# Kernel optimization log

Measured on AMD Instinct MI355X. Metric: run time of the kernel, lower is better.

## Reference

```python
import jax, jax.numpy as jnp
import numpy as np

EMB, HID, VOC, NLAYERS, TLEN = 256, 512, 32000, 2, 64
SRC_LEN, BS = 128, 64
DEC_HID = 2 * HID  # decoder hidden = hidden_dim * 2


def _p(key, shape, scale=0.05):
    return jax.random.normal(key, shape, dtype=jnp.float32) * scale


def setup_inputs() -> dict:
    key = jax.random.key(0)
    ks = jax.random.split(key, 24)
    d = {}
    d["sentences"] = jax.random.randint(ks[0], (SRC_LEN, BS), 0, VOC)
    d["targets"] = jax.random.randint(ks[1], (TLEN, BS), 0, VOC)
    d["emb"] = _p(ks[2], (VOC, EMB))
    # encoder: bidirectional, 2 layers; gate order i,f,g,o (PyTorch)
    d["enc0_Wih"] = _p(ks[3], (2, 4 * HID, EMB))
    d["enc0_Whh"] = _p(ks[4], (2, 4 * HID, HID))
    d["enc0_bih"] = _p(ks[5], (2, 4 * HID))
    d["enc0_bhh"] = _p(ks[6], (2, 4 * HID))
    d["enc1_Wih"] = _p(ks[7], (2, 4 * HID, 2 * HID))
    d["enc1_Whh"] = _p(ks[8], (2, 4 * HID, HID))
    d["enc1_bih"] = _p(ks[9], (2, 4 * HID))
    d["enc1_bhh"] = _p(ks[10], (2, 4 * HID))
    # decoder: unidirectional, 2 layers, hidden DEC_HID
    d["dec0_Wih"] = _p(ks[11], (4 * DEC_HID, EMB))
    d["dec0_Whh"] = _p(ks[12], (4 * DEC_HID, DEC_HID))
    d["dec0_bih"] = _p(ks[13], (4 * DEC_HID,))
    d["dec0_bhh"] = _p(ks[14], (4 * DEC_HID,))
    d["dec1_Wih"] = _p(ks[15], (4 * DEC_HID, DEC_HID))
    d["dec1_Whh"] = _p(ks[16], (4 * DEC_HID, DEC_HID))
    d["dec1_bih"] = _p(ks[17], (4 * DEC_HID,))
    d["dec1_bhh"] = _p(ks[18], (4 * DEC_HID,))
    d["W_out"] = _p(ks[19], (VOC, DEC_HID))
    d["b_out"] = _p(ks[20], (VOC,))
    return d


def lstm_scan(x, h0, c0, Wih, Whh, bih, bhh, reverse=False):
    # x: (T,B,In). Precompute input projection for the whole sequence.
    xw = jnp.einsum('tbi,gi->tbg', x, Wih) + bih  # (T,B,4H)

    def step(carry, g_in):
        h, c = carry
        g = g_in + h @ Whh.T + bhh
        i, f, gg, o = jnp.split(g, 4, axis=-1)
        c = jax.nn.sigmoid(f) * c + jax.nn.sigmoid(i) * jnp.tanh(gg)
        h = jax.nn.sigmoid(o) * jnp.tanh(c)
        return (h, c), h

    (hT, cT), ys = jax.lax.scan(step, (h0, c0), xw, reverse=reverse)
    return ys, hT, cT


def _forward(sentences, targets, emb,
             enc0_Wih, enc0_Whh, enc0_bih, enc0_bhh,
             enc1_Wih, enc1_Whh, enc1_bih, enc1_bhh,
             dec0_Wih, dec0_Whh, dec0_bih, dec0_bhh,
             dec1_Wih, dec1_Whh, dec1_bih, dec1_bhh,
             W_out, b_out):
    bs = sentences.shape[1]
    x = emb[sentences]  # (S,B,E)
    z = jnp.zeros((bs, HID), jnp.float32)
    enc_layers = ((enc0_Wih, enc0_Whh, enc0_bih, enc0_bhh),
                  (enc1_Wih, enc1_Whh, enc1_bih, enc1_bhh))
    hs, cs = [], []
    for Wih, Whh, bih, bhh in enc_layers:
        yf, hf, cf = lstm_scan(x, z, z, Wih[0], Whh[0], bih[0], bhh[0])
        yb, hb, cb = lstm_scan(x, z, z, Wih[1], Whh[1], bih[1], bhh[1], reverse=True)
        x = jnp.concatenate([yf, yb], axis=-1)  # (S,B,2H)
        hs.append(jnp.concatenate([hf, hb], axis=-1))  # _reshape_hidden concat
        cs.append(jnp.concatenate([cf, cb], axis=-1))
    # teacher forcing: decoder inputs are last source token, then targets[:-1]
    dec_tokens = jnp.concatenate([sentences[-1:], targets[:-1]], axis=0)  # (T,B)
    y = emb[dec_tokens]  # (T,B,E); dropout is identity in eval mode
    dec_layers = ((dec0_Wih, dec0_Whh, dec0_bih, dec0_bhh),
                  (dec1_Wih, dec1_Whh, dec1_bih, dec1_bhh))
    for l, (Wih, Whh, bih, bhh) in enumerate(dec_layers):
        y, _, _ = lstm_scan(y, hs[l], cs[l], Wih, Whh, bih, bhh)
    logits = jnp.einsum('tbh,vh->tbv', y, W_out) + b_out  # (T,B,V)
    return jax.nn.log_softmax(logits, axis=-1)


def reference(sentences, targets, emb,
              enc0_Wih, enc0_Whh, enc0_bih, enc0_bhh,
              enc1_Wih, enc1_Whh, enc1_bih, enc1_bhh,
              dec0_Wih, dec0_Whh, dec0_bih, dec0_bhh,
              dec1_Wih, dec1_Whh, dec1_bih, dec1_bhh,
              W_out, b_out):
    return _forward(sentences, targets, emb,
                    enc0_Wih, enc0_Whh, enc0_bih, enc0_bhh,
                    enc1_Wih, enc1_Whh, enc1_bih, enc1_bhh,
                    dec0_Wih, dec0_Whh, dec0_bih, dec0_bhh,
                    dec1_Wih, dec1_Whh, dec1_bih, dec1_bhh,
                    W_out, b_out)
```

## Files before the change

kernel.cpp:

```cpp
#include <hip/hip_runtime.h>

#define S_LEN 128
#define T_LEN 64
#define BSZ   64
#define EMBD  256
#define HID_  512
#define DHID_ 1024
#define VOC_  32000
#define HSTR  1024

typedef float  f4_t  __attribute__((ext_vector_type(4)));
typedef float  f32x4 __attribute__((ext_vector_type(4)));
typedef short  s16x8 __attribute__((ext_vector_type(8)));
typedef __bf16 bf16x8 __attribute__((ext_vector_type(8)));
typedef unsigned short u16x4 __attribute__((ext_vector_type(4)));
typedef int    i32x2 __attribute__((ext_vector_type(2)));

#define WS_XWA  0ull
#define WS_XWB  (WS_XWA + 16777216ull)
#define WS_CS   (WS_XWB + 16777216ull)
#define WS_BAR  (WS_CS  + 131072ull)
#define WS_BF   (WS_BAR + 32768ull)
#define U_X0B   0ull
#define U_HE0   (U_X0B + 2097152ull)
#define U_HE1   (U_HE0 + 8388608ull)
#define U_HD0   (U_HE1 + 8388608ull)
#define U_HD1   (U_HD0 + 4194304ull)
#define U_HSB   (U_HD1 + 4194304ull)
#define U_E0W   (U_HSB + 131072ull)
#define U_E1W   (U_E0W + 1048576ull)
#define U_D0W   (U_E1W + 4194304ull)
#define U_D1W   (U_D0W + 1048576ull)

__device__ __forceinline__ unsigned short f2bf(float x) {
    unsigned u = __builtin_bit_cast(unsigned, x);
    return (unsigned short)((u + 0x7fffu + ((u >> 16) & 1u)) >> 16);
}

__device__ __forceinline__ f4_t sc_load4(const void* p) {
    f4_t v;
    asm volatile("global_load_dwordx4 %0, %1, off sc0 sc1" : "=v"(v) : "v"(p));
    return v;
}
__device__ __forceinline__ int sc_load1(const int* p) {
    int v;
    asm volatile("global_load_dword %0, %1, off sc0 sc1\n\ts_waitcnt vmcnt(0)"
                 : "=v"(v) : "v"(p) : "memory");
    return v;
}
__device__ __forceinline__ void sc_store_int(int* p, int v) {
    asm volatile("global_store_dword %0, %1, off sc0 sc1" :: "v"(p), "v"(v) : "memory");
}
__device__ __forceinline__ void sc_store8(void* p, i32x2 v) {
    asm volatile("global_store_dwordx2 %0, %1, off sc0 sc1" :: "v"(p), "v"(v) : "memory");
}
__device__ __forceinline__ float g_load1(const float* p) {
    float v;
    asm volatile("global_load_dword %0, %1, off" : "=v"(v) : "v"(p));
    return v;
}
__device__ __forceinline__ void wait_vm0() {
    asm volatile("s_waitcnt vmcnt(0)" ::: "memory");
}
__device__ __forceinline__ void wait_vm8() {
    asm volatile("s_waitcnt vmcnt(8)" ::: "memory");
}

__device__ __forceinline__ void gload_lds16(const void* g, void* l) {
    __builtin_amdgcn_global_load_lds(
        (const __attribute__((address_space(1))) void*)g,
        (__attribute__((address_space(3))) void*)l, 16, 0, 0);
}

__device__ __forceinline__ float sigmoidf_(float x) { return 1.f / (1.f + expf(-x)); }

__global__ __launch_bounds__(256) void f2b_kernel(
    const float* __restrict__ in, unsigned short* __restrict__ out, int n4)
{
    const int stride = gridDim.x * 256;
    for (int i = blockIdx.x * 256 + threadIdx.x; i < n4; i += stride) {
        const float4 v = reinterpret_cast<const float4*>(in)[i];
        u16x4 o = { f2bf(v.x), f2bf(v.y), f2bf(v.z), f2bf(v.w) };
        reinterpret_cast<u16x4*>(out)[i] = o;
    }
}

__global__ __launch_bounds__(64) void embed_src_kernel(
    const int* __restrict__ toks, const float* __restrict__ emb,
    unsigned short* __restrict__ out)
{
    const int i = blockIdx.x;
    const int tok = toks[i];
    const float4 v = reinterpret_cast<const float4*>(emb + (size_t)tok * EMBD)[threadIdx.x];
    u16x4 o = { f2bf(v.x), f2bf(v.y), f2bf(v.z), f2bf(v.w) };
    reinterpret_cast<u16x4*>(out + (size_t)i * EMBD)[threadIdx.x] = o;
}

__global__ __launch_bounds__(64) void embed_dec_kernel(
    const int* __restrict__ sent, const int* __restrict__ targ,
    const float* __restrict__ emb, unsigned short* __restrict__ out)
{
    const int i = blockIdx.x;
    const int t = i >> 6, b = i & 63;
    const int tok = (t == 0) ? sent[(S_LEN - 1) * BSZ + b] : targ[(t - 1) * BSZ + b];
    const float4 v = reinterpret_cast<const float4*>(emb + (size_t)tok * EMBD)[threadIdx.x];
    u16x4 o = { f2bf(v.x), f2bf(v.y), f2bf(v.z), f2bf(v.w) };
    reinterpret_cast<u16x4*>(out + (size_t)i * EMBD)[threadIdx.x] = o;
}

__global__ __launch_bounds__(256) void gemm_bf16_kernel(
    const unsigned short* __restrict__ A, const unsigned short* __restrict__ B,
    const float* __restrict__ b1, const float* __restrict__ b2,
    float* __restrict__ C, int M, int N, int K, int nTN, int tmode)
{
    __shared__ __align__(16) unsigned short As[128 * 64];
    __shared__ __align__(16) unsigned short Bs[128 * 64];

    const int tid  = threadIdx.x;
    const int lane = tid & 63;
    const int wv   = tid >> 6;
    const int wm   = wv >> 1, wn = wv & 1;

    const int nwg = gridDim.x;
    const int q = nwg >> 3, r = nwg & 7;
    const int xcd = blockIdx.x & 7, io = blockIdx.x >> 3;
    const int wg = (xcd < r ? xcd * (q + 1) : r * (q + 1) + (xcd - r) * q) + io;
    const int bm = (wg / nTN) * 128;
    const int bn = (wg % nTN) * 128;

    f32x4 acc[4][4];
#pragma unroll
    for (int i = 0; i < 4; ++i)
#pragma unroll
        for (int j = 0; j < 4; ++j) acc[i][j] = (f32x4)0.f;

    const int lin_base = wv * 1024 + lane * 16;

    for (int k0 = 0; k0 < K; k0 += 64) {
        __syncthreads();
#pragma unroll
        for (int qc = 0; qc < 4; ++qc) {
            const int lin = qc * 4096 + lin_base;
            const int row = lin >> 7;
            const int c   = (lin >> 4) & 7;
            const int sc  = c ^ (row & 7);
            const size_t gofs  = (size_t)(bm + row) * K + k0 + sc * 8;
            const size_t gofsB = (size_t)(bn + row) * K + k0 + sc * 8;
            char* ldst  = (char*)As + qc * 4096 + wv * 1024;
            char* ldstB = (char*)Bs + qc * 4096 + wv * 1024;
            gload_lds16(A + gofs, ldst);
            gload_lds16(B + gofsB, ldstB);
        }
        asm volatile("s_waitcnt vmcnt(0)" ::: "memory");
        __syncthreads();
#pragma unroll
        for (int ks = 0; ks < 2; ++ks) {
            bf16x8 af[4], bfv[4];
            const int ca = ks * 4 + (lane >> 4);
#pragma unroll
            for (int f = 0; f < 4; ++f) {
                const int ra = wm * 64 + f * 16 + (lane & 15);
                af[f] = __builtin_bit_cast(bf16x8,
                    *(const s16x8*)((const char*)As + ra * 128 + ((ca ^ (ra & 7)) << 4)));
                const int rb = wn * 64 + f * 16 + (lane & 15);
                bfv[f] = __builtin_bit_cast(bf16x8,
                    *(const s16x8*)((const char*)Bs + rb * 128 + ((ca ^ (rb & 7)) << 4)));
            }
#pragma unroll
            for (int i = 0; i < 4; ++i)
#pragma unroll
                for (int j = 0; j < 4; ++j)
                    acc[i][j] = __builtin_amdgcn_mfma_f32_16x16x32_bf16(
                        af[i], bfv[j], acc[i][j], 0, 0, 0);
        }
    }

    const int col0 = bn + wn * 64 + (lane & 15);
    if (tmode == 0) {
        const int row0 = bm + wm * 64 + ((lane >> 4) << 2);
#pragma unroll
        for (int i = 0; i < 4; ++i) {
#pragma unroll
            for (int j = 0; j < 4; ++j) {
                const int col = col0 + j * 16;
                float bias = b1[col];
                if (b2) bias += b2[col];
#pragma unroll
                for (int rg = 0; rg < 4; ++rg)
                    C[(size_t)(row0 + i * 16 + rg) * N + col] = acc[i][j][rg] + bias;
            }
        }
    } else {
        const int tblk = (bm >> 6) + wm;
        const int rb = (lane >> 4) << 2;
#pragma unroll
        for (int i = 0; i < 4; ++i) {
#pragma unroll
            for (int j = 0; j < 4; ++j) {
                const int col = col0 + j * 16;
                float bias = b1[col];
                if (b2) bias += b2[col];
                float4 v = { acc[i][j][0] + bias, acc[i][j][1] + bias,
                             acc[i][j][2] + bias, acc[i][j][3] + bias };
                *reinterpret_cast<float4*>(&C[((size_t)tblk * N + col) * 64 + rb + i * 16]) = v;
            }
        }
    }
}

template<int H_T>
__global__ __launch_bounds__(256, 1) void lstm_mfma_scan(
    const float* __restrict__ xw0, const float* __restrict__ xw1,
    const float* __restrict__ Whh0, const float* __restrict__ Whh1,
    const unsigned short* __restrict__ h0b, const float* __restrict__ c0,
    unsigned short* __restrict__ hist,
    unsigned short* __restrict__ hsb, float* __restrict__ csd,
    int T, int ndir, int rev_mask, int* bar)
{
    constexpr int KST = H_T / 32;
    constexpr int CH  = H_T / 8;
    constexpr int NB  = (64 * CH) / 2048;

    __shared__ __align__(16) unsigned short h_lds[64 * H_T];
    __shared__ float pre[64][17];
    __shared__ __align__(8) unsigned short hpack[64][4];

    const int tid  = threadIdx.x;
    const int lane = tid & 63;
    const int w    = tid >> 6;
    const int bpd  = (ndir == 2) ? 128 : 256;
    const int dir  = blockIdx.x / bpd;
    const int blk  = blockIdx.x - dir * bpd;
    const int m0   = blk * 4;
    const int rev  = (rev_mask >> dir) & 1;
    const float* xw  = dir ? xw1  : xw0;
    const float* Whh = dir ? Whh1 : Whh0;
    const int dcol = dir * H_T;
    const int b = tid & 63;
    const int j = tid >> 6;

    int* myflag = bar + blockIdx.x * 32;
    const int* pollflag = bar + (dir * bpd + (tid < bpd ? tid : 0)) * 32;
    const bool polls = (tid < bpd);

    const int n  = lane & 15;
    const int kg = lane >> 4;
    const int wr = (n >> 2) * H_T + m0 + (n & 3);
    s16x8 wfr[KST];
#pragma unroll
    for (int ks = 0; ks < KST; ++ks) {
        const float* wp = Whh + (size_t)wr * H_T + ks * 32 + kg * 8;
        const float4 lo = *reinterpret_cast<const float4*>(wp);
        const float4 hi = *reinterpret_cast<const float4*>(wp + 4);
        s16x8 rr;
        rr[0] = (short)f2bf(lo.x); rr[1] = (short)f2bf(lo.y);
        rr[2] = (short)f2bf(lo.z); rr[3] = (short)f2bf(lo.w);
        rr[4] = (short)f2bf(hi.x); rr[5] = (short)f2bf(hi.y);
        rr[6] = (short)f2bf(hi.z); rr[7] = (short)f2bf(hi.w);
        wfr[ks] = rr;
    }

    float c  = c0 ? c0[(size_t)b * HSTR + dcol + m0 + j] : 0.f;
    float hn = 0.f;
    const int rA  = w * 16 + n;
    const int rAx = rA & 7;

    for (int s = 0; s < T; ++s) {
        const int tt = rev ? (T - 1 - s) : s;

        const float* xb = xw + ((size_t)tt * (4 * H_T) + m0 + j) * 64 + b;
        float xg0 = g_load1(xb);
        float xg1 = g_load1(xb + (size_t)H_T * 64);
        float xg2 = g_load1(xb + (size_t)2 * H_T * 64);
        float xg3 = g_load1(xb + (size_t)3 * H_T * 64);

        if (s > 0) {
            int ok = polls ? 0 : 1;
            for (;;) {
                if (!ok) ok = (sc_load1(pollflag) >= s) ? 1 : 0;
                if (__syncthreads_and(ok)) break;
            }
        }

        const unsigned short* hb;
        size_t tofs;
        if (s == 0) { hb = h0b; tofs = 0; }
        else {
            const int tp = rev ? (tt + 1) : (tt - 1);
            hb = hist; tofs = (size_t)tp * (64 * 1024);
        }

        float p0 = 0.f, p1 = 0.f, p2 = 0.f, p3 = 0.f;
        if (hb) {
            f4_t bufA[8], bufB[8];
            auto issue = [&](f4_t (&bf)[8], int bt) {
#pragma unroll
                for (int jj = 0; jj < 8; ++jj) {
                    const int idx = (bt * 8 + jj) * 256 + tid;
                    const int rr_ = idx / CH, cc_ = idx % CH;
                    bf[jj] = sc_load4(hb + tofs + (size_t)rr_ * 1024 + dcol + cc_ * 8);
                }
            };
            auto writeb = [&](const f4_t (&bf)[8], int bt) {
#pragma unroll
                for (int jj = 0; jj < 8; ++jj) {
                    const int idx = (bt * 8 + jj) * 256 + tid;
                    const int rr_ = idx / CH, cc_ = idx % CH;
                    const int off = rr_ * (2 * H_T) + ((cc_ ^ (rr_ & 7)) << 4);
                    *(f4_t*)((char*)h_lds + off) = bf[jj];
                }
            };
            issue(bufA, 0);
            if (NB > 1) issue(bufB, 1);
#pragma unroll
            for (int bt = 0; bt < NB; ++bt) {
                if (bt + 1 < NB) wait_vm8(); else wait_vm0();
                if (bt & 1) writeb(bufB, bt); else writeb(bufA, bt);
                if (bt + 2 < NB) { if (bt & 1) issue(bufB, bt + 2); else issue(bufA, bt + 2); }
            }
            __syncthreads();

            f32x4 acc = {0.f, 0.f, 0.f, 0.f};
#pragma unroll
            for (int ks = 0; ks < KST; ++ks) {
                const int cc_ = ks * 4 + kg;
                const int off = rA * (2 * H_T) + ((cc_ ^ rAx) << 4);
                const bf16x8 a = __builtin_bit_cast(bf16x8,
                    *(const s16x8*)((const char*)h_lds + off));
                acc = __builtin_amdgcn_mfma_f32_16x16x32_bf16(
                    a, __builtin_bit_cast(bf16x8, wfr[ks]), acc, 0, 0, 0);
            }
            __syncthreads();
#pragma unroll
            for (int rg = 0; rg < 4; ++rg)
                pre[w * 16 + kg * 4 + rg][n] = acc[rg];
            __syncthreads();
            p0 = pre[b][0 + j]; p1 = pre[b][4 + j];
            p2 = pre[b][8 + j]; p3 = pre[b][12 + j];
        }

        asm volatile("s_waitcnt vmcnt(0)"
                     : "+v"(xg0), "+v"(xg1), "+v"(xg2), "+v"(xg3) :: "memory");

        const float ig = sigmoidf_(p0 + xg0);
        const float fg = sigmoidf_(p1 + xg1);
        const float gg = tanhf(p2 + xg2);
        const float og = sigmoidf_(p3 + xg3);
        c  = fg * c + ig * gg;
        hn = og * tanhf(c);

        hpack[b][j] = f2bf(hn);
        __syncthreads();
        if (tid < 64) {
            const i32x2 v2 = *reinterpret_cast<const i32x2*>(&hpack[tid][0]);
            sc_store8(hist + (size_t)tt * (64 * 1024) + (size_t)tid * 1024 + dcol + m0, v2);
        }
        wait_vm0();
        __syncthreads();
        if (s + 1 < T && tid == 0) sc_store_int(myflag, s + 1);
    }

    if (hsb) hsb[(size_t)b * 1024 + dcol + m0 + j] = f2bf(hn);
    if (csd) csd[(size_t)b * HSTR + dcol + m0 + j] = c;
}

__global__ __launch_bounds__(256) void logsoftmax_kernel(float* __restrict__ x, int n4)
{
    __shared__ __align__(16) float row[VOC_];
    __shared__ float ms[256], ss[256];
    const int tid = threadIdx.x;
    float4* p = reinterpret_cast<float4*>(x + (size_t)blockIdx.x * (n4 * 4));
    float m = -3.0e38f, s = 0.f;
    for (int cc = tid; cc < n4; cc += 256) {
        const float4 v = p[cc];
        *reinterpret_cast<float4*>(&row[cc * 4]) = v;
        const float vv[4] = { v.x, v.y, v.z, v.w };
#pragma unroll
        for (int e = 0; e < 4; ++e) {
            const float z = vv[e];
            if (z > m) { s = s * expf(m - z) + 1.f; m = z; }
            else       { s += expf(z - m); }
        }
    }
    ms[tid] = m; ss[tid] = s;
    __syncthreads();
    for (int off = 128; off > 0; off >>= 1) {
        if (tid < off) {
            const float m2 = ms[tid + off], s2 = ss[tid + off];
            const float m1 = ms[tid],       s1 = ss[tid];
            const float M = fmaxf(m1, m2);
            ss[tid] = s1 * expf(m1 - M) + s2 * expf(m2 - M);
            ms[tid] = M;
        }
        __syncthreads();
    }
    const float ML = ms[0] + logf(ss[0]);
    for (int cc = tid; cc < n4; cc += 256) {
        float4 v = *reinterpret_cast<const float4*>(&row[cc * 4]);
        v.x -= ML; v.y -= ML; v.z -= ML; v.w -= ML;
        p[cc] = v;
    }
}

extern "C" void kernel_launch(void* const* d_in, const int* in_sizes, int n_in,
                              void* d_out, int out_size, void* d_ws, size_t ws_size,
                              hipStream_t stream)
{
    const int*   sent  = (const int*)d_in[0];
    const int*   targ  = (const int*)d_in[1];
    const float* emb   = (const float*)d_in[2];
    const float* e0Wih = (const float*)d_in[3];
    const float* e0Whh = (const float*)d_in[4];
    const float* e0bih = (const float*)d_in[5];
    const float* e0bhh = (const float*)d_in[6];
    const float* e1Wih = (const float*)d_in[7];
    const float* e1Whh = (const float*)d_in[8];
    const float* e1bih = (const float*)d_in[9];
    const float* e1bhh = (const float*)d_in[10];
    const float* d0Wih = (const float*)d_in[11];
    const float* d0Whh = (const float*)d_in[12];
    const float* d0bih = (const float*)d_in[13];
    const float* d0bhh = (const float*)d_in[14];
    const float* d1Wih = (const float*)d_in[15];
    const float* d1Whh = (const float*)d_in[16];
    const float* d1bih = (const float*)d_in[17];
    const float* d1bhh = (const float*)d_in[18];
    const float* Wout  = (const float*)d_in[19];
    const float* bout  = (const float*)d_in[20];

    float* ws  = (float*)d_ws;
    float* xwA = ws + WS_XWA;
    float* xwB = ws + WS_XWB;
    float* cs  = ws + WS_CS;
    int*   bar = (int*)(ws + WS_BAR);
    unsigned short* ub    = (unsigned short*)(ws + WS_BF);
    unsigned short* x0b   = ub + U_X0B;
    unsigned short* h_e0  = ub + U_HE0;
    unsigned short* h_e1  = ub + U_HE1;
    unsigned short* h_d0  = ub + U_HD0;
    unsigned short* h_d1  = ub + U_HD1;
    unsigned short* hsb   = ub + U_HSB;
    unsigned short* e0Wb  = ub + U_E0W;
    unsigned short* e1Wb  = ub + U_E1W;
    unsigned short* d0Wb  = ub + U_D0W;
    unsigned short* d1Wb  = ub + U_D1W;
    unsigned short* Woutb = (unsigned short*)xwA;
    float* out = (float*)d_out;

    hipMemsetAsync(bar, 0, 4 * 8192 * sizeof(int), stream);

    f2b_kernel<<<256, 256, 0, stream>>>(e0Wih, e0Wb, 1048576 / 4);
    f2b_kernel<<<512, 256, 0, stream>>>(e1Wih, e1Wb, 4194304 / 4);
    f2b_kernel<<<256, 256, 0, stream>>>(d0Wih, d0Wb, 1048576 / 4);
    f2b_kernel<<<512, 256, 0, stream>>>(d1Wih, d1Wb, 4194304 / 4);

    embed_src_kernel<<<S_LEN * BSZ, 64, 0, stream>>>(sent, emb, x0b);
    gemm_bf16_kernel<<<64 * 16, 256, 0, stream>>>(x0b, e0Wb, e0bih, e0bhh, xwA,
                                                  S_LEN * BSZ, 2048, EMBD, 16, 1);
    gemm_bf16_kernel<<<64 * 16, 256, 0, stream>>>(x0b, e0Wb + 2048ull * 256,
                                                  e0bih + 2048, e0bhh + 2048, xwB,
                                                  S_LEN * BSZ, 2048, EMBD, 16, 1);
    lstm_mfma_scan<512><<<256, 256, 0, stream>>>(xwA, xwB, e0Whh, e0Whh + 2048ull * 512,
                                                 nullptr, nullptr, h_e0,
                                                 hsb, cs, S_LEN, 2, 2, bar);
    gemm_bf16_kernel<<<64 * 16, 256, 0, stream>>>(h_e0, e1Wb, e1bih, e1bhh, xwA,
                                                  S_LEN * BSZ, 2048, 2 * HID_, 16, 1);
    gemm_bf16_kernel<<<64 * 16, 256, 0, stream>>>(h_e0, e1Wb + 2048ull * 1024,
                                                  e1bih + 2048, e1bhh + 2048, xwB,
                                                  S_LEN * BSZ, 2048, 2 * HID_, 16, 1);
    lstm_mfma_scan<512><<<256, 256, 0, stream>>>(xwA, xwB, e1Whh, e1Whh + 2048ull * 512,
                                                 nullptr, nullptr, h_e1,
                                                 hsb + 65536, cs + 65536,
                                                 S_LEN, 2, 2, bar + 8192);
    embed_dec_kernel<<<T_LEN * BSZ, 64, 0, stream>>>(sent, targ, emb, x0b);
    gemm_bf16_kernel<<<32 * 32, 256, 0, stream>>>(x0b, d0Wb, d0bih, d0bhh, xwA,
                                                  T_LEN * BSZ, 4 * DHID_, EMBD, 32, 1);
    lstm_mfma_scan<1024><<<256, 256, 0, stream>>>(xwA, nullptr, d0Whh, nullptr,
                                                  hsb, cs, h_d0,
                                                  nullptr, nullptr, T_LEN, 1, 0,
                                                  bar + 2 * 8192);
    f2b_kernel<<<2048, 256, 0, stream>>>(Wout, Woutb, (VOC_ * DHID_) / 4);
    gemm_bf16_kernel<<<32 * 32, 256, 0, stream>>>(h_d0, d1Wb, d1bih, d1bhh, xwB,
                                                  T_LEN * BSZ, 4 * DHID_, DHID_, 32, 1);
    lstm_mfma_scan<1024><<<256, 256, 0, stream>>>(xwB, nullptr, d1Whh, nullptr,
                                                  hsb + 65536, cs + 65536, h_d1,
                                                  nullptr, nullptr, T_LEN, 1, 0,
                                                  bar + 3 * 8192);
    gemm_bf16_kernel<<<32 * 250, 256, 0, stream>>>(h_d1, Woutb, bout, nullptr, out,
                                                   T_LEN * BSZ, VOC_, DHID_, 250, 0);
    logsoftmax_kernel<<<T_LEN * BSZ, 256, 0, stream>>>(out, VOC_ / 4);
}
```

Measured before the change: 2.959 ms.

## Fuse log-softmax partial reductions into output GEMM epilogue and merge encoder GEMMs

The vocab projection GEMM epilogue now computes a per-tile row max and sum-exp and writes them to a partials buffer. A small merge kernel combines the 250 partials per row, and a normalize kernel subtracts the log-sum-exp in place, so the separate pass that rereads the whole 32000-wide logits row for the reductions is gone. The two direction GEMMs of each encoder layer are also merged into a single launch with N=4096, and the scan addresses both directions through a fixed 4096 stride. The cost is extra shuffles and expf work in the GEMM epilogue, one extra kernel launch, and reuse of the xwB and cs buffers as scratch.

Measured after the change: 2.679 ms. -9.5%, faster.

```diff
diff --git a/kernel.cpp b/kernel.cpp
--- a/kernel.cpp
+++ b/kernel.cpp
@@ -111,10 +111,12 @@
 __global__ __launch_bounds__(256) void gemm_bf16_kernel(
     const unsigned short* __restrict__ A, const unsigned short* __restrict__ B,
     const float* __restrict__ b1, const float* __restrict__ b2,
-    float* __restrict__ C, int M, int N, int K, int nTN, int tmode)
+    float* __restrict__ C, int M, int N, int K, int nTN, int tmode,
+    float* __restrict__ part)
 {
     __shared__ __align__(16) unsigned short As[128 * 64];
     __shared__ __align__(16) unsigned short Bs[128 * 64];
+    __shared__ float prt[2][128][2];
 
     const int tid  = threadIdx.x;
     const int lane = tid & 63;
@@ -178,16 +180,75 @@
     const int col0 = bn + wn * 64 + (lane & 15);
     if (tmode == 0) {
         const int row0 = bm + wm * 64 + ((lane >> 4) << 2);
-#pragma unroll
-        for (int i = 0; i < 4; ++i) {
-#pragma unroll
-            for (int j = 0; j < 4; ++j) {
-                const int col = col0 + j * 16;
-                float bias = b1[col];
-                if (b2) bias += b2[col];
+        float bs[4];
+#pragma unroll
+        for (int j = 0; j < 4; ++j) {
+            const int col = col0 + j * 16;
+            bs[j] = b1[col];
+            if (b2) bs[j] += b2[col];
+        }
+#pragma unroll
+        for (int i = 0; i < 4; ++i)
+#pragma unroll
+            for (int j = 0; j < 4; ++j)
 #pragma unroll
                 for (int rg = 0; rg < 4; ++rg)
-                    C[(size_t)(row0 + i * 16 + rg) * N + col] = acc[i][j][rg] + bias;
+                    C[(size_t)(row0 + i * 16 + rg) * N + col0 + j * 16] = acc[i][j][rg] + bs[j];
+
+        if (part) {
+            float pm[4][4], ps[4][4];
+#pragma unroll
+            for (int i = 0; i < 4; ++i)
+#pragma unroll
+                for (int rg = 0; rg < 4; ++rg) {
+                    float m = acc[i][0][rg] + bs[0];
+                    m = fmaxf(m, acc[i][1][rg] + bs[1]);
+                    m = fmaxf(m, acc[i][2][rg] + bs[2]);
+                    m = fmaxf(m, acc[i][3][rg] + bs[3]);
+                    pm[i][rg] = m;
+                }
+#pragma unroll
+            for (int mask = 1; mask <= 8; mask <<= 1)
+#pragma unroll
+                for (int i = 0; i < 4; ++i)
+#pragma unroll
+                    for (int rg = 0; rg < 4; ++rg)
+                        pm[i][rg] = fmaxf(pm[i][rg], __shfl_xor(pm[i][rg], mask));
+#pragma unroll
+            for (int i = 0; i < 4; ++i)
+#pragma unroll
+                for (int rg = 0; rg < 4; ++rg) {
+                    float s = 0.f;
+#pragma unroll
+                    for (int j = 0; j < 4; ++j)
+                        s += expf(acc[i][j][rg] + bs[j] - pm[i][rg]);
+                    ps[i][rg] = s;
+                }
+#pragma unroll
+            for (int mask = 1; mask <= 8; mask <<= 1)
+#pragma unroll
+                for (int i = 0; i < 4; ++i)
+#pragma unroll
+                    for (int rg = 0; rg < 4; ++rg)
+                        ps[i][rg] += __shfl_xor(ps[i][rg], mask);
+            if ((lane & 15) == 0) {
+#pragma unroll
+                for (int i = 0; i < 4; ++i)
+#pragma unroll
+                    for (int rg = 0; rg < 4; ++rg) {
+                        const int r64 = ((lane >> 4) << 2) + i * 16 + rg;
+                        prt[wn][wm * 64 + r64][0] = pm[i][rg];
+                        prt[wn][wm * 64 + r64][1] = ps[i][rg];
+                    }
+            }
+            __syncthreads();
+            if (tid < 128) {
+                const float m0_ = prt[0][tid][0], s0_ = prt[0][tid][1];
+                const float m1_ = prt[1][tid][0], s1_ = prt[1][tid][1];
+                const float Mx = fmaxf(m0_, m1_);
+                const float Sx = s0_ * expf(m0_ - Mx) + s1_ * expf(m1_ - Mx);
+                const size_t o = ((size_t)(bm + tid) * nTN + (bn >> 7)) * 2;
+                part[o] = Mx; part[o + 1] = Sx;
             }
         }
     } else {
@@ -268,7 +329,7 @@
     for (int s = 0; s < T; ++s) {
         const int tt = rev ? (T - 1 - s) : s;
 
-        const float* xb = xw + ((size_t)tt * (4 * H_T) + m0 + j) * 64 + b;
+        const float* xb = xw + ((size_t)tt * 4096 + m0 + j) * 64 + b;
         float xg0 = g_load1(xb);
         float xg1 = g_load1(xb + (size_t)H_T * 64);
         float xg2 = g_load1(xb + (size_t)2 * H_T * 64);
@@ -364,23 +425,18 @@
     if (csd) csd[(size_t)b * HSTR + dcol + m0 + j] = c;
 }
 
-__global__ __launch_bounds__(256) void logsoftmax_kernel(float* __restrict__ x, int n4)
-{
-    __shared__ __align__(16) float row[VOC_];
+__global__ __launch_bounds__(256) void lsm_merge_kernel(
+    const float* __restrict__ part, float* __restrict__ ml, int nt)
+{
     __shared__ float ms[256], ss[256];
     const int tid = threadIdx.x;
-    float4* p = reinterpret_cast<float4*>(x + (size_t)blockIdx.x * (n4 * 4));
     float m = -3.0e38f, s = 0.f;
-    for (int cc = tid; cc < n4; cc += 256) {
-        const float4 v = p[cc];
-        *reinterpret_cast<float4*>(&row[cc * 4]) = v;
-        const float vv[4] = { v.x, v.y, v.z, v.w };
-#pragma unroll
-        for (int e = 0; e < 4; ++e) {
-            const float z = vv[e];
-            if (z > m) { s = s * expf(m - z) + 1.f; m = z; }
-            else       { s += expf(z - m); }
-        }
+    for (int t = tid; t < nt; t += 256) {
+        const float mo = part[((size_t)blockIdx.x * nt + t) * 2];
+        const float so = part[((size_t)blockIdx.x * nt + t) * 2 + 1];
+        const float M = fmaxf(m, mo);
+        s = s * expf(m - M) + so * expf(mo - M);
+        m = M;
     }
     ms[tid] = m; ss[tid] = s;
     __syncthreads();
@@ -394,9 +450,16 @@
         }
         __syncthreads();
     }
-    const float ML = ms[0] + logf(ss[0]);
-    for (int cc = tid; cc < n4; cc += 256) {
-        float4 v = *reinterpret_cast<const float4*>(&row[cc * 4]);
+    if (tid == 0) ml[blockIdx.x] = ms[0] + logf(ss[0]);
+}
+
+__global__ __launch_bounds__(256) void lsm_norm_kernel(
+    float* __restrict__ x, const float* __restrict__ ml, int n4)
+{
+    const float ML = ml[blockIdx.x];
+    float4* p = reinterpret_cast<float4*>(x + (size_t)blockIdx.x * (n4 * 4));
+    for (int cc = threadIdx.x; cc < n4; cc += 256) {
+        float4 v = p[cc];
         v.x -= ML; v.y -= ML; v.z -= ML; v.w -= ML;
         p[cc] = v;
     }
@@ -446,6 +509,7 @@
     unsigned short* d1Wb  = ub + U_D1W;
     unsigned short* Woutb = (unsigned short*)xwA;
     float* out = (float*)d_out;
+    float* ml  = cs;
 
     hipMemsetAsync(bar, 0, 4 * 8192 * sizeof(int), stream);
 
@@ -455,38 +519,35 @@
     f2b_kernel<<<512, 256, 0, stream>>>(d1Wih, d1Wb, 4194304 / 4);
 
     embed_src_kernel<<<S_LEN * BSZ, 64, 0, stream>>>(sent, emb, x0b);
-    gemm_bf16_kernel<<<64 * 16, 256, 0, stream>>>(x0b, e0Wb, e0bih, e0bhh, xwA,
-                                                  S_LEN * BSZ, 2048, EMBD, 16, 1);
-    gemm_bf16_kernel<<<64 * 16, 256, 0, stream>>>(x0b, e0Wb + 2048ull * 256,
-                                                  e0bih + 2048, e0bhh + 2048, xwB,
-                                                  S_LEN * BSZ, 2048, EMBD, 16, 1);
-    lstm_mfma_scan<512><<<256, 256, 0, stream>>>(xwA, xwB, e0Whh, e0Whh + 2048ull * 512,
+    gemm_bf16_kernel<<<64 * 32, 256, 0, stream>>>(x0b, e0Wb, e0bih, e0bhh, xwA,
+                                                  S_LEN * BSZ, 4096, EMBD, 32, 1, nullptr);
+    lstm_mfma_scan<512><<<256, 256, 0, stream>>>(xwA, xwA + 2048 * 64,
+                                                 e0Whh, e0Whh + 2048ull * 512,
                                                  nullptr, nullptr, h_e0,
                                                  hsb, cs, S_LEN, 2, 2, bar);
-    gemm_bf16_kernel<<<64 * 16, 256, 0, stream>>>(h_e0, e1Wb, e1bih, e1bhh, xwA,
-                                                  S_LEN * BSZ, 2048, 2 * HID_, 16, 1);
-    gemm_bf16_kernel<<<64 * 16, 256, 0, stream>>>(h_e0, e1Wb + 2048ull * 1024,
-                                                  e1bih + 2048, e1bhh + 2048, xwB,
-                                                  S_LEN * BSZ, 2048, 2 * HID_, 16, 1);
-    lstm_mfma_scan<512><<<256, 256, 0, stream>>>(xwA, xwB, e1Whh, e1Whh + 2048ull * 512,
+    gemm_bf16_kernel<<<64 * 32, 256, 0, stream>>>(h_e0, e1Wb, e1bih, e1bhh, xwA,
+                                                  S_LEN * BSZ, 4096, 2 * HID_, 32, 1, nullptr);
+    lstm_mfma_scan<512><<<256, 256, 0, stream>>>(xwA, xwA + 2048 * 64,
+                                                 e1Whh, e1Whh + 2048ull * 512,
                                                  nullptr, nullptr, h_e1,
                                                  hsb + 65536, cs + 65536,
                                                  S_LEN, 2, 2, bar + 8192);
     embed_dec_kernel<<<T_LEN * BSZ, 64, 0, stream>>>(sent, targ, emb, x0b);
     gemm_bf16_kernel<<<32 * 32, 256, 0, stream>>>(x0b, d0Wb, d0bih, d0bhh, xwA,
-                                                  T_LEN * BSZ, 4 * DHID_, EMBD, 32, 1);
+                                                  T_LEN * BSZ, 4 * DHID_, EMBD, 32, 1, nullptr);
     lstm_mfma_scan<1024><<<256, 256, 0, stream>>>(xwA, nullptr, d0Whh, nullptr,
                                                   hsb, cs, h_d0,
                                                   nullptr, nullptr, T_LEN, 1, 0,
                                                   bar + 2 * 8192);
     f2b_kernel<<<2048, 256, 0, stream>>>(Wout, Woutb, (VOC_ * DHID_) / 4);
     gemm_bf16_kernel<<<32 * 32, 256, 0, stream>>>(h_d0, d1Wb, d1bih, d1bhh, xwB,
-                                                  T_LEN * BSZ, 4 * DHID_, DHID_, 32, 1);
+                                                  T_LEN * BSZ, 4 * DHID_, DHID_, 32, 1, nullptr);
     lstm_mfma_scan<1024><<<256, 256, 0, stream>>>(xwB, nullptr, d1Whh, nullptr,
                                                   hsb + 65536, cs + 65536, h_d1,
                                                   nullptr, nullptr, T_LEN, 1, 0,
                                                   bar + 3 * 8192);
     gemm_bf16_kernel<<<32 * 250, 256, 0, stream>>>(h_d1, Woutb, bout, nullptr, out,
-                                                   T_LEN * BSZ, VOC_, DHID_, 250, 0);
-    logsoftmax_kernel<<<T_LEN * BSZ, 256, 0, stream>>>(out, VOC_ / 4);
-}
+                                                   T_LEN * BSZ, VOC_, DHID_, 250, 0, xwB);
+    lsm_merge_kernel<<<T_LEN * BSZ, 256, 0, stream>>>(xwB, ml, 250);
+    lsm_norm_kernel<<<T_LEN * BSZ, 256, 0, stream>>>(out, ml, VOC_ / 4);
+}
```
